# Kernel optimization log

Measured on AMD Instinct MI355X. Metric: run time of the kernel, lower is better.

Reference implementation:

```python
import jax, jax.numpy as jnp
import numpy as np

H, W = 32, 32          # input_resolution
N = H * W
DIM = 256
DG = 128               # dim_group
NG = DIM // DG         # num_groups = 2
NH = 8                 # num_heads
DH = DIM // NH         # dim_head = 32
NHG = NH // NG         # heads per group = 4
KS = 5                 # offset kernel size
FACTOR = 2.0           # offset_range_factor
EPS = 1e-5


def get_reference(h, w):
    ry = jnp.linspace(0.5, h - 0.5, h) / h * 2.0 - 1.0
    rx = jnp.linspace(0.5, w - 0.5, w) / w * 2.0 - 1.0
    gy, gx = jnp.meshgrid(ry, rx, indexing='ij')
    return jnp.stack((gy, gx), axis=-1)  # [h, w, 2] = (y, x) in [-1, 1]


def grid_sample(img, grid):
    # torch F.grid_sample: bilinear, align_corners=True, padding_mode='zeros'
    # img: [B, C, Hi, Wi]; grid: [B, ..., 2] with (x, y) in [-1, 1]
    B, C, Hi, Wi = img.shape
    gs = grid.shape[1:-1]
    x = (grid[..., 0] + 1.0) * 0.5 * (Wi - 1)
    y = (grid[..., 1] + 1.0) * 0.5 * (Hi - 1)
    x0 = jnp.floor(x)
    y0 = jnp.floor(y)
    imgf = img.reshape(B, C, Hi * Wi)
    out = jnp.zeros((B, C, int(np.prod(gs))), img.dtype)
    for dy in (0, 1):
        for dx in (0, 1):
            yi = y0 + dy
            xi = x0 + dx
            wgt = (1.0 - jnp.abs(x - xi)) * (1.0 - jnp.abs(y - yi))
            valid = (yi >= 0) & (yi < Hi) & (xi >= 0) & (xi < Wi)
            yc = jnp.clip(yi, 0, Hi - 1).astype(jnp.int32)
            xc = jnp.clip(xi, 0, Wi - 1).astype(jnp.int32)
            idx = (yc * Wi + xc).reshape(B, 1, -1)
            g = jnp.take_along_axis(imgf, jnp.broadcast_to(idx, (B, C, idx.shape[-1])), axis=2)
            out = out + g * (wgt * valid).reshape(B, 1, -1)
    return out.reshape(B, C, *gs)


def setup_inputs() -> dict:
    key = jax.random.key(0)
    ks = jax.random.split(key, 10)
    s = 0.02
    return {
        'x': jax.random.normal(ks[0], (8, N, DIM), jnp.float32),
        'Wq': jax.random.normal(ks[1], (DIM, DIM), jnp.float32) * s,
        'Wkv': jax.random.normal(ks[2], (DIM, 2 * DIM), jnp.float32) * s,
        'conv_w': jax.random.normal(ks[3], (DG, 1, KS, KS), jnp.float32) * s,   # depthwise OIHW
        'conv_b': jnp.zeros((DG,), jnp.float32),
        'ln_g': jnp.ones((DG,), jnp.float32),
        'ln_b': jnp.zeros((DG,), jnp.float32),
        'Woff': jax.random.normal(ks[4], (DG, 2), jnp.float32) * s,
        'rpe': jax.random.normal(ks[5], (NH, 2 * H - 1, 2 * W - 1), jnp.float32) * 0.01,
        'Wout': jax.random.normal(ks[6], (DIM, DIM), jnp.float32) * s,
        'bout': jnp.zeros((DIM,), jnp.float32),
    }


def reference(x, Wq, Wkv, conv_w, conv_b, ln_g, ln_b, Woff, rpe, Wout, bout):
    B = x.shape[0]
    scale = DH ** (-0.5)
    ref = get_reference(H, W)  # [H, W, 2] (y, x)

    q = x @ Wq  # [B, N, DIM]

    # rearrange 'b (h w) (ng dg) -> (b ng) dg h w'
    xg = q.reshape(B, H, W, NG, DG).transpose(0, 3, 4, 1, 2).reshape(B * NG, DG, H, W)

    # conv_offset: depthwise conv -> LN -> GELU -> Linear(dg, 2)
    off = jax.lax.conv_general_dilated(
        xg, conv_w, (1, 1), [(KS // 2, KS // 2)] * 2,
        dimension_numbers=('NCHW', 'OIHW', 'NCHW'), feature_group_count=DG)
    off = off + conv_b[None, :, None, None]
    off = off.transpose(0, 2, 3, 1)  # [Bng, H, W, DG]
    mu = off.mean(-1, keepdims=True)
    var = ((off - mu) ** 2).mean(-1, keepdims=True)
    off = (off - mu) * jax.lax.rsqrt(var + EPS) * ln_g + ln_b
    off = jax.nn.gelu(off, approximate=False)
    offset = off @ Woff  # [Bng, H, W, 2] (y, x)
    offset = jnp.tanh(offset) * jnp.array([1.0 / H, 1.0 / W], jnp.float32) * FACTOR

    pos = offset + ref  # [Bng, H, W, 2] (y, x)

    # deformable sampling of q-feature map
    x_sampled = grid_sample(xg, pos[..., ::-1])  # [Bng, DG, H, W]
    # '(b ng) dg h w -> b (h w) (ng dg)'
    x_sampled = x_sampled.reshape(B, NG, DG, H * W).transpose(0, 3, 1, 2).reshape(B, N, NG * DG)

    # relative-position-bias lookup via grid_sample
    rpe_bias = jnp.broadcast_to(rpe.reshape(1, NG, NHG, 2 * H - 1, 2 * W - 1),
                                (B, NG, NHG, 2 * H - 1, 2 * W - 1)).reshape(B * NG, NHG, 2 * H - 1, 2 * W - 1)
    q_grid = ref.reshape(1, N, 1, 2)
    posr = pos.reshape(B * NG, 1, N, 2)
    disp = (q_grid - posr) * 0.5  # [Bng, N, N, 2]
    attn_bias = grid_sample(rpe_bias, disp[..., ::-1])  # [Bng, NHG, N, N]
    attn_bias = attn_bias.reshape(B, NG * NHG, N, N)     # [B, NH, N, N]

    kv = x_sampled @ Wkv
    k, v = kv[..., :DIM], kv[..., DIM:]
    qh = q.reshape(B, N, NH, DH).transpose(0, 2, 1, 3) * scale
    kh = k.reshape(B, N, NH, DH).transpose(0, 2, 1, 3)
    vh = v.reshape(B, N, NH, DH).transpose(0, 2, 1, 3)

    sim = jnp.einsum('bhid,bhjd->bhij', qh, kh) + attn_bias
    attn = jax.nn.softmax(sim, axis=-1)
    out = jnp.einsum('bhij,bhjd->bhid', attn, vh)
    out = out.transpose(0, 2, 1, 3).reshape(B, N, NH * DH)
    return out @ Wout + bout
```

## Files before the change

kernel.cpp:

```cpp
#include <hip/hip_runtime.h>
#include <hip/hip_bf16.h>
#include <hip/hip_fp16.h>
#include <hip/hip_fp8.h>


#define EPS_ 1e-5f
#define ASCALE 0.17677669529663687f
#define LOG2E  1.4426950408889634f

typedef __attribute__((ext_vector_type(8))) short bf16x8;
typedef __attribute__((ext_vector_type(4))) float f32x4;

__device__ __forceinline__ short f2bf(float f) {
  union { float f; unsigned u; } v; v.f = f;
  unsigned r = (v.u + 0x7fffu + ((v.u >> 16) & 1u)) >> 16;
  return (short)r;
}
__device__ __forceinline__ unsigned pk2bf(float a, float b) {
  union { __hip_bfloat162 h; unsigned u; } v;
  v.h = __float22bfloat162_rn(make_float2(a, b));
  return v.u;
}
__device__ __forceinline__ float exp2_fast(float x) {
  return __builtin_amdgcn_exp2f(x);
}

__global__ __launch_bounds__(256) void prep_weights(
    const float* __restrict__ Wkv, const float* __restrict__ Wout,
    const float* __restrict__ Wq, short* __restrict__ Wkvt,
    short* __restrict__ Woutt, short* __restrict__ Wqt)
{
  int bid = blockIdx.x, k = threadIdx.x;
  if (bid < 512) Wkvt[bid * 256 + k] = f2bf(Wkv[k * 512 + bid]);
  else if (bid < 768) { int n = bid - 512; Woutt[n * 256 + k] = f2bf(Wout[k * 256 + n]); }
  else { int n = bid - 768; Wqt[n * 256 + k] = f2bf(Wq[k * 256 + n]); }
}

__global__ __launch_bounds__(256) void gemm_bf16(
    const short* __restrict__ Ab, const float* __restrict__ Af,
    const short* __restrict__ Bt,
    float* __restrict__ Cf, short* __restrict__ Cb,
    const float* __restrict__ bias, int N)
{
  __shared__ __align__(16) short As[64 * 40];
  __shared__ __align__(16) short Bs[64 * 40];
  const int t = threadIdx.x;
  const int n0 = blockIdx.x << 6, m0 = blockIdx.y << 6;
  const int wv = t >> 6, l16 = t & 15, quad = (t & 63) >> 4;
  const int row = t >> 2, koff = (t & 3) << 3;

  auto loadA = [&](int k0) -> bf16x8 {
    if (Af) {
      const float* src = &Af[(size_t)(m0 + row) * 256 + k0 + koff];
      float4 f0 = *(const float4*)src;
      float4 f1 = *(const float4*)(src + 4);
      union { unsigned u[4]; bf16x8 v; } c;
      c.u[0] = pk2bf(f0.x, f0.y); c.u[1] = pk2bf(f0.z, f0.w);
      c.u[2] = pk2bf(f1.x, f1.y); c.u[3] = pk2bf(f1.z, f1.w);
      return c.v;
    }
    return *(const bf16x8*)&Ab[(size_t)(m0 + row) * 256 + k0 + koff];
  };

  f32x4 acc[4] = {};
  bf16x8 av = loadA(0);
  bf16x8 bv = *(const bf16x8*)&Bt[(size_t)(n0 + row) * 256 + koff];
  for (int k0 = 0; k0 < 256; k0 += 32) {
    __syncthreads();
    *(bf16x8*)&As[row * 40 + koff] = av;
    *(bf16x8*)&Bs[row * 40 + koff] = bv;
    __syncthreads();
    if (k0 + 32 < 256) {
      av = loadA(k0 + 32);
      bv = *(const bf16x8*)&Bt[(size_t)(n0 + row) * 256 + k0 + 32 + koff];
    }
    bf16x8 a = *(const bf16x8*)&As[((wv << 4) + l16) * 40 + (quad << 3)];
#pragma unroll
    for (int jt = 0; jt < 4; jt++) {
      bf16x8 bb = *(const bf16x8*)&Bs[((jt << 4) + l16) * 40 + (quad << 3)];
      acc[jt] = __builtin_amdgcn_mfma_f32_16x16x32_bf16(a, bb, acc[jt], 0, 0, 0);
    }
  }
#pragma unroll
  for (int jt = 0; jt < 4; jt++) {
#pragma unroll
    for (int r = 0; r < 4; r++) {
      int mrow = m0 + (wv << 4) + (quad << 2) + r;
      int ncol = n0 + (jt << 4) + l16;
      float v = acc[jt][r];
      if (bias) v += bias[ncol];
      if (Cf) Cf[(size_t)mrow * N + ncol] = v;
      else    Cb[(size_t)mrow * N + ncol] = f2bf(v);
    }
  }
}

__global__ __launch_bounds__(256) void conv_pos_sample_kernel(
    const float* __restrict__ q, const float* __restrict__ conv_w,
    const float* __restrict__ conv_b, const float* __restrict__ ln_g,
    const float* __restrict__ ln_b, const float* __restrict__ Woff,
    float* __restrict__ pos, short* __restrict__ xsb)
{
  const int p = (blockIdx.x << 2) + (threadIdx.x >> 6);
  const int lane = threadIdx.x & 63;
  const int bg = p >> 10, pix = p & 1023;
  const int hh = pix >> 5, ww = pix & 31;
  const int b = bg >> 1, g = bg & 1;
  const int c0 = lane << 1;

  float2 cb = *(const float2*)&conv_b[c0];
  float a0 = cb.x, a1 = cb.y;
  const float* w0 = conv_w + c0 * 25;
  const float* w1 = w0 + 25;
#pragma unroll
  for (int dy = 0; dy < 5; dy++) {
    int y = hh + dy - 2;
    if ((unsigned)y < 32u) {
#pragma unroll
      for (int dx = 0; dx < 5; dx++) {
        int x = ww + dx - 2;
        if ((unsigned)x < 32u) {
          float2 qv = *(const float2*)&q[(size_t)((b << 10) + (y << 5) + x) * 256 + (g << 7) + c0];
          a0 = fmaf(qv.x, w0[dy * 5 + dx], a0);
          a1 = fmaf(qv.y, w1[dy * 5 + dx], a1);
        }
      }
    }
  }
  float s1 = a0 + a1, s2 = a0 * a0 + a1 * a1;
#pragma unroll
  for (int o = 32; o; o >>= 1) { s1 += __shfl_xor(s1, o); s2 += __shfl_xor(s2, o); }
  float mu = s1 * (1.f / 128.f);
  float inv = rsqrtf(fmaf(-mu, mu, s2 * (1.f / 128.f)) + EPS_);
  float2 lg = *(const float2*)&ln_g[c0];
  float2 lb = *(const float2*)&ln_b[c0];
  float v0 = (a0 - mu) * inv * lg.x + lb.x;
  float v1 = (a1 - mu) * inv * lg.y + lb.y;
  float ge0 = 0.5f * v0 * (1.f + erff(v0 * 0.70710678118654752f));
  float ge1 = 0.5f * v1 * (1.f + erff(v1 * 0.70710678118654752f));
  float2 W0 = *(const float2*)&Woff[c0 * 2];
  float2 W1 = *(const float2*)&Woff[c0 * 2 + 2];
  float o0 = ge0 * W0.x + ge1 * W1.x;
  float o1 = ge0 * W0.y + ge1 * W1.y;
#pragma unroll
  for (int o = 32; o; o >>= 1) { o0 += __shfl_xor(o0, o); o1 += __shfl_xor(o1, o); }
  float py = tanhf(o0) * 0.0625f + ((hh + 0.5f) * 0.0625f - 1.f);
  float px = tanhf(o1) * 0.0625f + ((ww + 0.5f) * 0.0625f - 1.f);
  if (lane == 0)
    ((float2*)pos)[(bg << 10) + pix] = make_float2(py, px);

  float x = (px + 1.f) * 15.5f;
  float y = (py + 1.f) * 15.5f;
  float x0f = floorf(x), y0f = floorf(y);
  int ix0 = (int)x0f, iy0 = (int)y0f;
  float fx = x - x0f, fy = y - y0f;
  float ac0 = 0.f, ac1 = 0.f;
#pragma unroll
  for (int dy = 0; dy < 2; dy++) {
#pragma unroll
    for (int dx = 0; dx < 2; dx++) {
      int yi = iy0 + dy, xi = ix0 + dx;
      float w = (dy ? fy : 1.f - fy) * (dx ? fx : 1.f - fx);
      if ((unsigned)yi < 32u && (unsigned)xi < 32u) {
        float2 qv = *(const float2*)&q[(size_t)((b << 10) + (yi << 5) + xi) * 256 + (g << 7) + c0];
        ac0 = fmaf(w, qv.x, ac0);
        ac1 = fmaf(w, qv.y, ac1);
      }
    }
  }
  *(unsigned*)&xsb[(size_t)((b << 10) + pix) * 256 + (g << 7) + c0] = pk2bf(ac0, ac1);
}

__global__ __launch_bounds__(256, 4) void attn_kernel(
    const float* __restrict__ q, const short* __restrict__ kvb,
    const float* __restrict__ pos, const float* __restrict__ rpe,
    short* __restrict__ ao)
{
  const int it = blockIdx.x, h = blockIdx.y, b = blockIdx.z;
  const int g = h >> 2, t = threadIdx.x;
  const int wv = t >> 6, l16 = t & 15, quad = (t & 63) >> 4;

  __shared__ __align__(16) short PL[64 * 72];
  __shared__ __align__(16) short Vt[32 * 68];
  __shared__ float2 posT[64];
  __shared__ __align__(16) unsigned rpe8[64 * 64];

  {
    const float* rp = rpe + h * 3969;
    for (int i = t; i < 4096; i += 256) {
      int ty = i >> 6, tx = i & 63;
      float v00 = 0.f, v10 = 0.f, v01 = 0.f, v11 = 0.f;
      if (tx <= 62) {
        if (ty <= 62) v00 = rp[ty * 63 + tx] * LOG2E;
        if (ty <= 61) v10 = rp[(ty + 1) * 63 + tx] * LOG2E;
      }
      if (tx <= 61) {
        if (ty <= 62) v01 = rp[ty * 63 + tx + 1] * LOG2E;
        if (ty <= 61) v11 = rp[(ty + 1) * 63 + tx + 1] * LOG2E;
      }
      __hip_fp8x2_e4m3 elo(make_float2(v00, v10));
      __hip_fp8x2_e4m3 ehi(make_float2(v01, v11));
      rpe8[i] = (unsigned)(unsigned short)elo.__x |
                ((unsigned)(unsigned short)ehi.__x << 16);
    }
  }

  const int row0 = (it << 6) + (wv << 4);
  bf16x8 aq;
  {
    const float* src = q + (size_t)((b << 10) + row0 + l16) * 256 + (h << 5) + (quad << 3);
    float4 f0 = *(const float4*)src;
    float4 f1 = *(const float4*)(src + 4);
    const float sc = ASCALE * LOG2E;
    union { unsigned u[4]; bf16x8 v; } c;
    c.u[0] = pk2bf(f0.x * sc, f0.y * sc); c.u[1] = pk2bf(f0.z * sc, f0.w * sc);
    c.u[2] = pk2bf(f1.x * sc, f1.y * sc); c.u[3] = pk2bf(f1.z * sc, f1.w * sc);
    aq = c.v;
  }

  const float ayc = 15.5f * (((row0 >> 5) + 0.5f) * 0.0625f - 1.f) + 31.f;
  float ax[4];
#pragma unroll
  for (int r = 0; r < 4; r++) {
    int ix = (row0 & 31) + (quad << 2) + r;
    ax[r] = 15.5f * ((ix + 0.5f) * 0.0625f - 1.f) + 31.f;
  }

  bf16x8 vones;
#pragma unroll
  for (int i = 0; i < 8; i++) vones[i] = (short)0x3F80;

  const int vj = t & 63, vc = t >> 6;
  const short* vsrc = kvb + (size_t)((b << 10) + vj) * 512 + 256 + (h << 5) + (vc << 3);
  const short* ksrc = kvb + (size_t)((b << 10) + l16) * 512 + (h << 5) + (quad << 3);
  const float2* psrc = (const float2*)pos + (((b << 1) + g) << 10) + t;

  f32x4 Oacc[2] = {};
  f32x4 lacc = {};

  for (int kt = 0; kt < 16; kt++) {
    __syncthreads();
    {
      bf16x8 vv = *(const bf16x8*)vsrc;
#pragma unroll
      for (int k2 = 0; k2 < 8; k2++) Vt[((vc << 3) + k2) * 68 + vj] = vv[k2];
    }
    if (t < 64) {
      float2 pp = *psrc;
      posT[t] = make_float2(-15.5f * pp.x, -15.5f * pp.y);
    }
    __syncthreads();

    f32x4 S[4];
#pragma unroll
    for (int jt = 0; jt < 4; jt++) {
      bf16x8 bk = *(const bf16x8*)(ksrc + (size_t)jt * 8192);
      f32x4 z = {};
      S[jt] = __builtin_amdgcn_mfma_f32_16x16x32_bf16(aq, bk, z, 0, 0, 0);
    }

    float fyv[4];
    int ybv[4];
    float wyv[4];
#pragma unroll
    for (int jt = 0; jt < 4; jt++) {
      float2 bv = posT[(jt << 4) + l16];
      float ys = ayc + bv.x;
      float y0f = floorf(ys);
      fyv[jt] = ys - y0f;
      ybv[jt] = (int)y0f << 6;
      wyv[jt] = bv.y;
    }

    unsigned pu[4][2];
#pragma unroll
    for (int jt = 0; jt < 4; jt++) {
      float fy = fyv[jt];
      int ybase = ybv[jt];
      float pv[4];
#pragma unroll
      for (int r = 0; r < 4; r++) {
        float sx = ax[r] + wyv[jt];
        float x0f = floorf(sx);
        float fx = sx - x0f;
        unsigned u = rpe8[ybase + (int)x0f];
        __hip_fp8x2_e4m3 plo, phi;
        plo.__x = (__hip_fp8x2_storage_t)(unsigned short)(u & 0xffffu);
        phi.__x = (__hip_fp8x2_storage_t)(unsigned short)(u >> 16);
        float2 ga = (float2)plo;
        float2 gb = (float2)phi;
        float h0 = fmaf(fx, gb.x - ga.x, ga.x);
        float h1 = fmaf(fx, gb.y - ga.y, ga.y);
        float bias = fmaf(fy, h1 - h0, h0);
        pv[r] = exp2_fast(S[jt][r] + bias);
      }
      pu[jt][0] = pk2bf(pv[0], pv[1]);
      pu[jt][1] = pk2bf(pv[2], pv[3]);
    }

#pragma unroll
    for (int jt = 0; jt < 4; jt++) {
      int cb = (jt << 4) + l16;
      int rb = ((wv << 4) + (quad << 2)) * 72 + cb;
      PL[rb]       = (short)(pu[jt][0] & 0xffff);
      PL[rb + 72]  = (short)(pu[jt][0] >> 16);
      PL[rb + 144] = (short)(pu[jt][1] & 0xffff);
      PL[rb + 216] = (short)(pu[jt][1] >> 16);
    }
    bf16x8 pa0 = *(const bf16x8*)&PL[((wv << 4) + l16) * 72 + (quad << 3)];
    bf16x8 pa1 = *(const bf16x8*)&PL[((wv << 4) + l16) * 72 + 32 + (quad << 3)];
#pragma unroll
    for (int dt = 0; dt < 2; dt++) {
      bf16x8 vb0 = *(const bf16x8*)&Vt[((dt << 4) + l16) * 68 + (quad << 3)];
      bf16x8 vb1 = *(const bf16x8*)&Vt[((dt << 4) + l16) * 68 + 32 + (quad << 3)];
      Oacc[dt] = __builtin_amdgcn_mfma_f32_16x16x32_bf16(pa0, vb0, Oacc[dt], 0, 0, 0);
      Oacc[dt] = __builtin_amdgcn_mfma_f32_16x16x32_bf16(pa1, vb1, Oacc[dt], 0, 0, 0);
    }
    lacc = __builtin_amdgcn_mfma_f32_16x16x32_bf16(pa0, vones, lacc, 0, 0, 0);
    lacc = __builtin_amdgcn_mfma_f32_16x16x32_bf16(pa1, vones, lacc, 0, 0, 0);

    vsrc += 32768; ksrc += 32768; psrc += 64;
  }

#pragma unroll
  for (int r = 0; r < 4; r++) {
    float inv = 1.f / lacc[r];
    int row = row0 + (quad << 2) + r;
#pragma unroll
    for (int dt = 0; dt < 2; dt++) {
      ao[(size_t)((b << 10) + row) * 256 + (h << 5) + (dt << 4) + l16] =
          f2bf(Oacc[dt][r] * inv);
    }
  }
}

extern "C" void kernel_launch(void* const* d_in, const int* in_sizes, int n_in,
                              void* d_out, int out_size, void* d_ws, size_t ws_size,
                              hipStream_t stream) {
  (void)in_sizes; (void)n_in; (void)out_size; (void)ws_size;
  const float* x      = (const float*)d_in[0];
  const float* Wq     = (const float*)d_in[1];
  const float* Wkv    = (const float*)d_in[2];
  const float* conv_w = (const float*)d_in[3];
  const float* conv_b = (const float*)d_in[4];
  const float* ln_g   = (const float*)d_in[5];
  const float* ln_b   = (const float*)d_in[6];
  const float* Woff   = (const float*)d_in[7];
  const float* rpe    = (const float*)d_in[8];
  const float* Wout   = (const float*)d_in[9];
  const float* bout   = (const float*)d_in[10];
  float* out = (float*)d_out;

  float* ws    = (float*)d_ws;
  float* q     = ws;
  float* pos   = ws + 2097152;
  short* kvb   = (short*)(ws + 2129920);
  short* xsb   = (short*)(ws + 4227072);
  short* aob   = (short*)(ws + 5275648);
  short* Wkvt  = (short*)(ws + 6324224);
  short* Woutt = (short*)(ws + 6389760);
  short* Wqt   = (short*)(ws + 6422528);

  prep_weights<<<1024, 256, 0, stream>>>(Wkv, Wout, Wq, Wkvt, Woutt, Wqt);
  gemm_bf16<<<dim3(4, 128), 256, 0, stream>>>(nullptr, x, Wqt, q, nullptr, nullptr, 256);
  conv_pos_sample_kernel<<<4096, 256, 0, stream>>>(q, conv_w, conv_b, ln_g, ln_b,
                                                   Woff, pos, xsb);
  gemm_bf16<<<dim3(8, 128), 256, 0, stream>>>(xsb, nullptr, Wkvt, nullptr, kvb, nullptr, 512);
  attn_kernel<<<dim3(16, 8, 8), 256, 0, stream>>>(q, kvb, pos, rpe, aob);
  gemm_bf16<<<dim3(4, 128), 256, 0, stream>>>(aob, nullptr, Woutt, out, nullptr, bout, 256);
}
```

Before: 233.8 us.

## Split attention keys across two blocks with atomic accumulation and precomputed fp8 RPE table

Splits each attention block's 16 key tiles into two halves on separate blocks. The unnormalized outputs and row sums go into fp32 buffers via atomicAdd, and normalization moves into the A-load of the output GEMM. The fp8 RPE table is built once in a separate kernel that also zeroes the accumulators, and each attention block copies only a 36-row window of it into shared memory. The aim is to double grid parallelism and remove redundant per-block RPE conversion, at the cost of atomics, an extra launch, and an fp32 round trip through memory.

```diff
diff --git a/kernel.cpp b/kernel.cpp
--- a/kernel.cpp
+++ b/kernel.cpp
@@ -23,6 +23,36 @@
 }
 __device__ __forceinline__ float exp2_fast(float x) {
   return __builtin_amdgcn_exp2f(x);
+}
+
+__device__ __forceinline__ unsigned pack_fp8_quad(float v00, float v10,
+                                                  float v01, float v11) {
+#if __has_builtin(__builtin_amdgcn_cvt_pk_fp8_f32)
+  int r = 0;
+  r = __builtin_amdgcn_cvt_pk_fp8_f32(v00, v10, r, false);
+  r = __builtin_amdgcn_cvt_pk_fp8_f32(v01, v11, r, true);
+  return (unsigned)r;
+#else
+  __hip_fp8x2_e4m3 elo(make_float2(v00, v10));
+  __hip_fp8x2_e4m3 ehi(make_float2(v01, v11));
+  return (unsigned)(unsigned short)elo.__x |
+         ((unsigned)(unsigned short)ehi.__x << 16);
+#endif
+}
+__device__ __forceinline__ void unpack_fp8_quad(unsigned u, float& g00,
+                                                float& g10, float& g01,
+                                                float& g11) {
+#if __has_builtin(__builtin_amdgcn_cvt_pk_f32_fp8)
+  auto ga = __builtin_amdgcn_cvt_pk_f32_fp8((int)u, false);
+  auto gb = __builtin_amdgcn_cvt_pk_f32_fp8((int)u, true);
+  g00 = ga[0]; g10 = ga[1]; g01 = gb[0]; g11 = gb[1];
+#else
+  __hip_fp8x2_e4m3 plo, phi;
+  plo.__x = (__hip_fp8x2_storage_t)(unsigned short)(u & 0xffffu);
+  phi.__x = (__hip_fp8x2_storage_t)(unsigned short)(u >> 16);
+  float2 fa = (float2)plo, fb = (float2)phi;
+  g00 = fa.x; g10 = fa.y; g01 = fb.x; g11 = fb.y;
+#endif
 }
 
 __global__ __launch_bounds__(256) void prep_weights(
@@ -36,11 +66,40 @@
   else { int n = bid - 768; Wqt[n * 256 + k] = f2bf(Wq[k * 256 + n]); }
 }
 
+__global__ __launch_bounds__(256) void build_rpe8_zero(
+    const float* __restrict__ rpe, unsigned* __restrict__ rpeq,
+    float* __restrict__ Oaccum, float* __restrict__ laccum)
+{
+  int bid = blockIdx.x, t = threadIdx.x;
+  if (bid >= 2176) {
+    ((float4*)laccum)[(size_t)(bid - 2176) * 256 + t] = make_float4(0.f, 0.f, 0.f, 0.f);
+    return;
+  }
+  if (bid >= 128) {
+    ((float4*)Oaccum)[(size_t)(bid - 128) * 256 + t] = make_float4(0.f, 0.f, 0.f, 0.f);
+    return;
+  }
+  int i = bid * 256 + t;
+  int h = i >> 12, idx = i & 4095;
+  int ty = idx >> 6, tx = idx & 63;
+  const float* rp = rpe + h * 3969;
+  float v00 = 0.f, v10 = 0.f, v01 = 0.f, v11 = 0.f;
+  if (tx <= 62) {
+    if (ty <= 62) v00 = rp[ty * 63 + tx] * LOG2E;
+    if (ty <= 61) v10 = rp[(ty + 1) * 63 + tx] * LOG2E;
+  }
+  if (tx <= 61) {
+    if (ty <= 62) v01 = rp[ty * 63 + tx + 1] * LOG2E;
+    if (ty <= 61) v11 = rp[(ty + 1) * 63 + tx + 1] * LOG2E;
+  }
+  rpeq[i] = pack_fp8_quad(v00, v10, v01, v11);
+}
+
 __global__ __launch_bounds__(256) void gemm_bf16(
     const short* __restrict__ Ab, const float* __restrict__ Af,
     const short* __restrict__ Bt,
     float* __restrict__ Cf, short* __restrict__ Cb,
-    const float* __restrict__ bias, int N)
+    const float* __restrict__ bias, int N, const float* __restrict__ lrow)
 {
   __shared__ __align__(16) short As[64 * 40];
   __shared__ __align__(16) short Bs[64 * 40];
@@ -54,9 +113,11 @@
       const float* src = &Af[(size_t)(m0 + row) * 256 + k0 + koff];
       float4 f0 = *(const float4*)src;
       float4 f1 = *(const float4*)(src + 4);
+      float s = 1.f;
+      if (lrow) s = 1.f / lrow[(size_t)(m0 + row) * 8 + ((k0 + koff) >> 5)];
       union { unsigned u[4]; bf16x8 v; } c;
-      c.u[0] = pk2bf(f0.x, f0.y); c.u[1] = pk2bf(f0.z, f0.w);
-      c.u[2] = pk2bf(f1.x, f1.y); c.u[3] = pk2bf(f1.z, f1.w);
+      c.u[0] = pk2bf(f0.x * s, f0.y * s); c.u[1] = pk2bf(f0.z * s, f0.w * s);
+      c.u[2] = pk2bf(f1.x * s, f1.y * s); c.u[3] = pk2bf(f1.z * s, f1.w * s);
       return c.v;
     }
     return *(const bf16x8*)&Ab[(size_t)(m0 + row) * 256 + k0 + koff];
@@ -173,36 +234,26 @@
 
 __global__ __launch_bounds__(256, 4) void attn_kernel(
     const float* __restrict__ q, const short* __restrict__ kvb,
-    const float* __restrict__ pos, const float* __restrict__ rpe,
-    short* __restrict__ ao)
+    const float* __restrict__ pos, const unsigned* __restrict__ rpeq,
+    float* __restrict__ Oaccum, float* __restrict__ laccum)
 {
-  const int it = blockIdx.x, h = blockIdx.y, b = blockIdx.z;
+  const int it = blockIdx.x >> 1, half = blockIdx.x & 1;
+  const int h = blockIdx.y, b = blockIdx.z;
   const int g = h >> 2, t = threadIdx.x;
   const int wv = t >> 6, l16 = t & 15, quad = (t & 63) >> 4;
 
   __shared__ __align__(16) short PL[64 * 72];
   __shared__ __align__(16) short Vt[32 * 68];
   __shared__ float2 posT[64];
-  __shared__ __align__(16) unsigned rpe8[64 * 64];
+  __shared__ __align__(16) unsigned rpe8[36 * 64];
+
+  const float aycb = 15.5f * ((2 * it + 0.5f) * 0.0625f - 1.f) + 31.f;
+  int ylo = (int)floorf(aycb) - 16;
+  ylo = ylo < 0 ? 0 : (ylo > 28 ? 28 : ylo);
 
   {
-    const float* rp = rpe + h * 3969;
-    for (int i = t; i < 4096; i += 256) {
-      int ty = i >> 6, tx = i & 63;
-      float v00 = 0.f, v10 = 0.f, v01 = 0.f, v11 = 0.f;
-      if (tx <= 62) {
-        if (ty <= 62) v00 = rp[ty * 63 + tx] * LOG2E;
-        if (ty <= 61) v10 = rp[(ty + 1) * 63 + tx] * LOG2E;
-      }
-      if (tx <= 61) {
-        if (ty <= 62) v01 = rp[ty * 63 + tx + 1] * LOG2E;
-        if (ty <= 61) v11 = rp[(ty + 1) * 63 + tx + 1] * LOG2E;
-      }
-      __hip_fp8x2_e4m3 elo(make_float2(v00, v10));
-      __hip_fp8x2_e4m3 ehi(make_float2(v01, v11));
-      rpe8[i] = (unsigned)(unsigned short)elo.__x |
-                ((unsigned)(unsigned short)ehi.__x << 16);
-    }
+    const unsigned* src = rpeq + (h << 12) + (ylo << 6);
+    for (int i = t; i < 36 * 64; i += 256) rpe8[i] = src[i];
   }
 
   const int row0 = (it << 6) + (wv << 4);
@@ -230,15 +281,16 @@
 #pragma unroll
   for (int i = 0; i < 8; i++) vones[i] = (short)0x3F80;
 
+  const int kt0 = half << 3;
   const int vj = t & 63, vc = t >> 6;
-  const short* vsrc = kvb + (size_t)((b << 10) + vj) * 512 + 256 + (h << 5) + (vc << 3);
-  const short* ksrc = kvb + (size_t)((b << 10) + l16) * 512 + (h << 5) + (quad << 3);
-  const float2* psrc = (const float2*)pos + (((b << 1) + g) << 10) + t;
+  const short* vsrc = kvb + (size_t)((b << 10) + (kt0 << 6) + vj) * 512 + 256 + (h << 5) + (vc << 3);
+  const short* ksrc = kvb + (size_t)((b << 10) + (kt0 << 6) + l16) * 512 + (h << 5) + (quad << 3);
+  const float2* psrc = (const float2*)pos + (((b << 1) + g) << 10) + (kt0 << 6) + t;
 
   f32x4 Oacc[2] = {};
   f32x4 lacc = {};
 
-  for (int kt = 0; kt < 16; kt++) {
+  for (int kt = 0; kt < 8; kt++) {
     __syncthreads();
     {
       bf16x8 vv = *(const bf16x8*)vsrc;
@@ -268,7 +320,7 @@
       float ys = ayc + bv.x;
       float y0f = floorf(ys);
       fyv[jt] = ys - y0f;
-      ybv[jt] = (int)y0f << 6;
+      ybv[jt] = ((int)y0f - ylo) << 6;
       wyv[jt] = bv.y;
     }
 
@@ -284,13 +336,10 @@
         float x0f = floorf(sx);
         float fx = sx - x0f;
         unsigned u = rpe8[ybase + (int)x0f];
-        __hip_fp8x2_e4m3 plo, phi;
-        plo.__x = (__hip_fp8x2_storage_t)(unsigned short)(u & 0xffffu);
-        phi.__x = (__hip_fp8x2_storage_t)(unsigned short)(u >> 16);
-        float2 ga = (float2)plo;
-        float2 gb = (float2)phi;
-        float h0 = fmaf(fx, gb.x - ga.x, ga.x);
-        float h1 = fmaf(fx, gb.y - ga.y, ga.y);
+        float g00, g10, g01, g11;
+        unpack_fp8_quad(u, g00, g10, g01, g11);
+        float h0 = fmaf(fx, g01 - g00, g00);
+        float h1 = fmaf(fx, g11 - g10, g10);
         float bias = fmaf(fy, h1 - h0, h0);
         pv[r] = exp2_fast(S[jt][r] + bias);
       }
@@ -324,13 +373,13 @@
 
 #pragma unroll
   for (int r = 0; r < 4; r++) {
-    float inv = 1.f / lacc[r];
     int row = row0 + (quad << 2) + r;
-#pragma unroll
-    for (int dt = 0; dt < 2; dt++) {
-      ao[(size_t)((b << 10) + row) * 256 + (h << 5) + (dt << 4) + l16] =
-          f2bf(Oacc[dt][r] * inv);
-    }
+    size_t mb = (size_t)((b << 10) + row);
+#pragma unroll
+    for (int dt = 0; dt < 2; dt++)
+      atomicAdd(&Oaccum[mb * 256 + (h << 5) + (dt << 4) + l16], Oacc[dt][r]);
+    if (l16 == 0)
+      atomicAdd(&laccum[mb * 8 + h], lacc[r]);
   }
 }
 
@@ -351,21 +400,24 @@
   const float* bout   = (const float*)d_in[10];
   float* out = (float*)d_out;
 
-  float* ws    = (float*)d_ws;
-  float* q     = ws;
-  float* pos   = ws + 2097152;
-  short* kvb   = (short*)(ws + 2129920);
-  short* xsb   = (short*)(ws + 4227072);
-  short* aob   = (short*)(ws + 5275648);
-  short* Wkvt  = (short*)(ws + 6324224);
-  short* Woutt = (short*)(ws + 6389760);
-  short* Wqt   = (short*)(ws + 6422528);
+  float* ws       = (float*)d_ws;
+  float* q        = ws;
+  float* pos      = ws + 2097152;
+  short* kvb      = (short*)(ws + 2129920);
+  short* Wkvt     = (short*)(ws + 4227072);
+  short* Woutt    = (short*)(ws + 4292608);
+  short* Wqt      = (short*)(ws + 4325376);
+  unsigned* rpeq  = (unsigned*)(ws + 4358144);
+  float* laccum   = ws + 4390912;
+  short* xsb      = (short*)(ws + 4456448);
+  float* Oaccum   = ws + 4456448;
 
   prep_weights<<<1024, 256, 0, stream>>>(Wkv, Wout, Wq, Wkvt, Woutt, Wqt);
-  gemm_bf16<<<dim3(4, 128), 256, 0, stream>>>(nullptr, x, Wqt, q, nullptr, nullptr, 256);
+  gemm_bf16<<<dim3(4, 128), 256, 0, stream>>>(nullptr, x, Wqt, q, nullptr, nullptr, 256, nullptr);
   conv_pos_sample_kernel<<<4096, 256, 0, stream>>>(q, conv_w, conv_b, ln_g, ln_b,
                                                    Woff, pos, xsb);
-  gemm_bf16<<<dim3(8, 128), 256, 0, stream>>>(xsb, nullptr, Wkvt, nullptr, kvb, nullptr, 512);
-  attn_kernel<<<dim3(16, 8, 8), 256, 0, stream>>>(q, kvb, pos, rpe, aob);
-  gemm_bf16<<<dim3(4, 128), 256, 0, stream>>>(aob, nullptr, Woutt, out, nullptr, bout, 256);
-}
+  gemm_bf16<<<dim3(8, 128), 256, 0, stream>>>(xsb, nullptr, Wkvt, nullptr, kvb, nullptr, 512, nullptr);
+  build_rpe8_zero<<<2240, 256, 0, stream>>>(rpe, rpeq, Oaccum, laccum);
+  attn_kernel<<<dim3(32, 8, 8), 256, 0, stream>>>(q, kvb, pos, rpeq, Oaccum, laccum);
+  gemm_bf16<<<dim3(4, 128), 256, 0, stream>>>(nullptr, Oaccum, Woutt, out, nullptr, bout, 256, laccum);
+}
```

After: 244.2 us. +4.4%, slower.
